# Kernel optimization log

Hardware: AMD Instinct MI355X
Metric: run time of the kernel (lower is better)

The kernel has to match this reference:

```python
import jax, jax.numpy as jnp
import numpy as np

B, N, C, H = 2, 2048, 1024, 16
D = C // H


def setup_inputs() -> dict:
    key = jax.random.key(0)
    k1, k2, k3, k4 = jax.random.split(key, 4)
    q = jax.random.normal(k1, (B, N, C), dtype=jnp.float32)
    k = jax.random.normal(k2, (B, H, N, D), dtype=jnp.float32)
    v = jax.random.normal(k3, (B, H, N, D), dtype=jnp.float32)
    # nn.Linear(C, C): weight [out, in], kaiming-uniform-ish scale
    proj_w = jax.random.normal(k4, (C, C), dtype=jnp.float32) * (1.0 / np.sqrt(C))
    proj_b = jnp.zeros((C,), dtype=jnp.float32)
    return {"q": q, "k": k, "v": v, "proj_w": proj_w, "proj_b": proj_b}


def reference(q, k, v, proj_w, proj_b):
    b, n, c = q.shape
    # [b,n,c] -> [b,h,n,d]
    qh = q.reshape(b, n, H, D).transpose(0, 2, 1, 3)
    # NOTE: original module has NO 1/sqrt(d) scaling — kept faithful.
    atten = jnp.einsum("bhnd,bhmd->bhnm", qh, k)
    atten = jax.nn.softmax(atten, axis=-1)
    # dropout layers are identity at inference
    x = jnp.einsum("bhnm,bhmd->bhnd", atten, v)
    x = x.transpose(0, 2, 1, 3).reshape(b, n, c)
    x = x @ proj_w.T + proj_b
    return x
```

## Files before the change

kernel.cpp:

```cpp
#include <hip/hip_runtime.h>
#include <hip/hip_bf16.h>

#define NB 2
#define NN 2048
#define NC 1024
#define NH 16
#define ND 64
#define LOG2E 1.4426950408889634f
#define NSPLIT 2

typedef __attribute__((ext_vector_type(4))) float f32x4;
typedef __attribute__((ext_vector_type(16))) float f32x16;
typedef __attribute__((ext_vector_type(8))) short bf16x8;
typedef __attribute__((ext_vector_type(4))) unsigned short us4;
typedef __attribute__((ext_vector_type(8))) unsigned short us8;
typedef __attribute__((ext_vector_type(4))) unsigned int u32x4;

#define MFMA32 __builtin_amdgcn_mfma_f32_32x32x16_bf16
#define MFMA16 __builtin_amdgcn_mfma_f32_16x16x32_bf16

#if __has_builtin(__builtin_amdgcn_exp2f)
#define EX2(x) __builtin_amdgcn_exp2f(x)
#else
#define EX2(x) __builtin_exp2f(x)
#endif

__device__ __forceinline__ unsigned short f2bf(float f) {
    unsigned int u = __builtin_bit_cast(unsigned int, f);
    u = (u + 0x7FFFu + ((u >> 16) & 1u)) >> 16;
    return (unsigned short)u;
}
__device__ __forceinline__ float bf2f(unsigned short h) {
    return __builtin_bit_cast(float, (unsigned int)h << 16);
}
__device__ __forceinline__ unsigned short f2bf_hw(float f) {
    __hip_bfloat16 b = __float2bfloat16(f);
    unsigned short u;
    __builtin_memcpy(&u, &b, 2);
    return u;
}
__device__ __forceinline__ unsigned int pk2(float lo, float hi) {
    return (unsigned int)f2bf_hw(lo) | ((unsigned int)f2bf_hw(hi) << 16);
}

__global__ __launch_bounds__(256) void kvf_kernel(const float* __restrict__ k,
                                                  const float* __restrict__ v,
                                                  unsigned short* __restrict__ kf,
                                                  unsigned short* __restrict__ vf) {
    __shared__ float T[32][68];
    const int bh = blockIdx.y, c = blockIdx.x, t = threadIdx.x;
    {
        const int row = t >> 3;
        const int g = t & 7;
        const float* src = k + ((size_t)bh * NN + c * 32 + row) * ND + g * 8;
        f32x4 x0 = *reinterpret_cast<const f32x4*>(src);
        f32x4 x1 = *reinterpret_cast<const f32x4*>(src + 4);
        us8 h;
        #pragma unroll
        for (int j = 0; j < 4; ++j) {
            h[j] = f2bf(x0[j]);
            h[4 + j] = f2bf(x1[j]);
        }
        const size_t fo = ((size_t)bh * 64 + c) * 2048 + g * 256 + row * 8;
        *reinterpret_cast<us8*>(kf + fo) = h;
    }
    {
        const int row = t >> 3, d0 = (t & 7) * 8;
        const float* src = v + ((size_t)bh * NN + c * 32 + row) * ND + d0;
        f32x4 a = *reinterpret_cast<const f32x4*>(src);
        f32x4 b2 = *reinterpret_cast<const f32x4*>(src + 4);
        *reinterpret_cast<f32x4*>(&T[row][d0]) = a;
        *reinterpret_cast<f32x4*>(&T[row][d0 + 4]) = b2;
    }
    __syncthreads();
    {
        const int g2 = t >> 6, hi = (t >> 5) & 1, l31 = t & 31;
        const int ks2 = g2 & 1, dt = g2 >> 1;
        us8 r;
        #pragma unroll
        for (int j = 0; j < 8; ++j) r[j] = f2bf(T[ks2 * 16 + hi * 8 + j][dt * 32 + l31]);
        const size_t fo = ((size_t)bh * 64 + c) * 2048 + (g2 * 2 + hi) * 256 + l31 * 8;
        *reinterpret_cast<us8*>(vf + fo) = r;
    }
}

__global__ __launch_bounds__(256) void wf_kernel(const float* __restrict__ w,
                                                 unsigned short* __restrict__ wf) {
    const int tid = blockIdx.x * 256 + threadIdx.x;
    const int ot = tid >> 11;
    const int s = tid & 2047;
    const int cc = s >> 6;
    const int lane = s & 63;
    const int l15 = lane & 15, lhi = lane >> 4;
    const float* src = w + (size_t)(ot * 16 + l15) * NC + cc * 32 + lhi * 8;
    f32x4 x0 = *reinterpret_cast<const f32x4*>(src);
    f32x4 x1 = *reinterpret_cast<const f32x4*>(src + 4);
    us8 r;
    #pragma unroll
    for (int j = 0; j < 4; ++j) {
        r[j] = f2bf(x0[j]);
        r[4 + j] = f2bf(x1[j]);
    }
    *reinterpret_cast<us8*>(wf + (size_t)tid * 8) = r;
}

#define ATTN_STEP(KC, KN, VC, VN, CI, CN)                                              \
    {                                                                                  \
        _Pragma("unroll")                                                              \
        for (int ks = 0; ks < 4; ++ks)                                                 \
            KN[ks] = *reinterpret_cast<const bf16x8*>(Kp + (CN) * 2048 + ks * 512);    \
        _Pragma("unroll")                                                              \
        for (int g = 0; g < 4; ++g)                                                    \
            VN[g] = *reinterpret_cast<const bf16x8*>(Vp + (CN) * 2048 + g * 512);      \
        f32x16 sa;                                                                     \
        _Pragma("unroll")                                                              \
        for (int r = 0; r < 16; ++r) sa[r] = 0.f;                                      \
        _Pragma("unroll")                                                              \
        for (int ks = 0; ks < 4; ++ks) sa = MFMA32(KC[ks], qh[ks], sa, 0, 0, 0);       \
        _Pragma("unroll")                                                              \
        for (int r = 0; r < 16; r += 4) {                                              \
            float e0 = EX2(sa[r]);                                                     \
            float e1 = EX2(sa[r + 1]);                                                 \
            float e2 = EX2(sa[r + 2]);                                                 \
            float e3 = EX2(sa[r + 3]);                                                 \
            sa[r] = e0; sa[r + 1] = e1; sa[r + 2] = e2; sa[r + 3] = e3;                \
            rs0 += e0; rs1 += e1; rs2 += e2; rs3 += e3;                                \
        }                                                                              \
        _Pragma("unroll")                                                              \
        for (int ks2 = 0; ks2 < 2; ++ks2) {                                            \
            unsigned int sA = pk2(sa[8 * ks2 + 0], sa[8 * ks2 + 1]);                   \
            unsigned int sB = pk2(sa[8 * ks2 + 2], sa[8 * ks2 + 3]);                   \
            unsigned int sC = pk2(sa[8 * ks2 + 4], sa[8 * ks2 + 5]);                   \
            unsigned int sD = pk2(sa[8 * ks2 + 6], sa[8 * ks2 + 7]);                   \
            unsigned int snd0 = hi ? sA : sC;                                          \
            unsigned int snd1 = hi ? sB : sD;                                          \
            unsigned int rcv0 = __shfl_xor(snd0, 32);                                  \
            unsigned int rcv1 = __shfl_xor(snd1, 32);                                  \
            u32x4 uf;                                                                  \
            uf[0] = hi ? rcv0 : sA;                                                    \
            uf[1] = hi ? rcv1 : sB;                                                    \
            uf[2] = hi ? sC : rcv0;                                                    \
            uf[3] = hi ? sD : rcv1;                                                    \
            bf16x8 pfrag = __builtin_bit_cast(bf16x8, uf);                             \
            if (ks2 == 0) {                                                            \
                acc0 = MFMA32(VC[0], pfrag, acc0, 0, 0, 0);                            \
                acc1 = MFMA32(VC[2], pfrag, acc1, 0, 0, 0);                            \
            } else {                                                                   \
                acc0 = MFMA32(VC[1], pfrag, acc0, 0, 0, 0);                            \
                acc1 = MFMA32(VC[3], pfrag, acc1, 0, 0, 0);                            \
            }                                                                          \
        }                                                                              \
    }

__global__ __launch_bounds__(256, 2) void attn_kernel(const float* __restrict__ q,
                                                      const unsigned short* __restrict__ kf,
                                                      const unsigned short* __restrict__ vf,
                                                      unsigned short* __restrict__ po,
                                                      float* __restrict__ pl) {
    const size_t X_ELEMS = (size_t)NB * NN * NC;
    const size_t ML_ELEMS = (size_t)NB * NN * NH;
    const int bid = blockIdx.x;
    const int swz = (bid & 7) * 128 + (bid >> 3);
    const int bh = swz >> 5;
    const int qt = (swz & 31) >> 1;
    const int split = swz & 1;
    const int b = bh >> 4, h = bh & 15;
    const int wave = threadIdx.x >> 6, lane = threadIdx.x & 63;
    const int l31 = lane & 31, hi = lane >> 5;
    const int qrow = qt * 128 + wave * 32 + l31;

    bf16x8 qh[4];
    {
        const float* qp = q + ((size_t)(b * NN + qrow)) * NC + h * ND;
        #pragma unroll
        for (int ks = 0; ks < 4; ++ks) {
            int d = ks * 16 + hi * 8;
            f32x4 x0 = *reinterpret_cast<const f32x4*>(qp + d);
            f32x4 x1 = *reinterpret_cast<const f32x4*>(qp + d + 4);
            bf16x8 ah;
            #pragma unroll
            for (int j = 0; j < 4; ++j) {
                ah[j] = (short)f2bf_hw(x0[j] * LOG2E);
                ah[4 + j] = (short)f2bf_hw(x1[j] * LOG2E);
            }
            qh[ks] = ah;
        }
    }

    f32x16 acc0, acc1;
    #pragma unroll
    for (int r = 0; r < 16; ++r) { acc0[r] = 0.f; acc1[r] = 0.f; }
    float rs0 = 0.f, rs1 = 0.f, rs2 = 0.f, rs3 = 0.f;

    const unsigned short* Kp = kf + (size_t)(bh * 64 + split * 32) * 2048 + hi * 256 + l31 * 8;
    const unsigned short* Vp = vf + (size_t)(bh * 64 + split * 32) * 2048 + hi * 256 + l31 * 8;

    bf16x8 kA[4], kB[4], vA[4], vB[4];
    #pragma unroll
    for (int ks = 0; ks < 4; ++ks) {
        kA[ks] = *reinterpret_cast<const bf16x8*>(Kp + ks * 512);
        vA[ks] = *reinterpret_cast<const bf16x8*>(Vp + ks * 512);
    }

    for (int ci = 0; ci < 32; ci += 2) {
        ATTN_STEP(kA, kB, vA, vB, ci, ci + 1)
        const int cn2 = (ci < 30) ? ci + 2 : 31;
        ATTN_STEP(kB, kA, vB, vA, ci + 1, cn2)
    }

    float rs = (rs0 + rs1) + (rs2 + rs3);
    rs += __shfl_xor(rs, 32);
    const float inv = 1.0f / rs;

    unsigned short* pob = po + (size_t)split * X_ELEMS;
    float* plb = pl + (size_t)split * ML_ELEMS;
    const int el15 = l31 & 15;
    const int nt = b * 128 + qt * 8 + wave * 2 + (l31 >> 4);
    #pragma unroll
    for (int dt = 0; dt < 2; ++dt) {
        const f32x16 a = (dt == 0) ? acc0 : acc1;
        unsigned int P0 = pk2(a[0] * inv, a[1] * inv);
        unsigned int P1 = pk2(a[2] * inv, a[3] * inv);
        unsigned int P2 = pk2(a[4] * inv, a[5] * inv);
        unsigned int P3 = pk2(a[6] * inv, a[7] * inv);
        unsigned int P4 = pk2(a[8] * inv, a[9] * inv);
        unsigned int P5 = pk2(a[10] * inv, a[11] * inv);
        unsigned int P6 = pk2(a[12] * inv, a[13] * inv);
        unsigned int P7 = pk2(a[14] * inv, a[15] * inv);
        unsigned int r0 = __shfl_xor(hi ? P0 : P4, 32);
        unsigned int r1 = __shfl_xor(hi ? P1 : P5, 32);
        unsigned int r2 = __shfl_xor(hi ? P2 : P6, 32);
        unsigned int r3 = __shfl_xor(hi ? P3 : P7, 32);
        u32x4 c0, c1;
        c0[0] = hi ? r0 : P0;
        c0[1] = hi ? r1 : P1;
        c0[2] = hi ? P4 : r0;
        c0[3] = hi ? P5 : r1;
        c1[0] = hi ? r2 : P2;
        c1[1] = hi ? r3 : P3;
        c1[2] = hi ? P6 : r2;
        c1[3] = hi ? P7 : r3;
        unsigned short* base = pob + (size_t)(nt * 32 + h * 2 + dt) * 512;
        *reinterpret_cast<u32x4*>(base + (hi * 32 + el15) * 8) = c0;
        *reinterpret_cast<u32x4*>(base + (hi * 32 + 16 + el15) * 8) = c1;
    }
    if (hi == 0) {
        plb[(size_t)(b * NN + qrow) * NH + h] = rs;
    }
}

__global__ __launch_bounds__(256) void combine_kernel(const unsigned short* __restrict__ po,
                                                      const float* __restrict__ pl,
                                                      unsigned short* __restrict__ xf) {
    const size_t X_ELEMS = (size_t)NB * NN * NC;
    const size_t ML_ELEMS = (size_t)NB * NN * NH;
    const int tid = blockIdx.x * 256 + threadIdx.x;
    const int nt = tid >> 10;
    const int v = tid & 1023;
    const int h = v >> 6;
    const int lane = v & 63;
    const int row = nt * 16 + (lane & 15);
    float w[NSPLIT];
    {
        float lsum = 0.f;
        #pragma unroll
        for (int i = 0; i < NSPLIT; ++i) {
            w[i] = pl[(size_t)i * ML_ELEMS + (size_t)row * NH + h];
            lsum += w[i];
        }
        float inv = 1.0f / lsum;
        #pragma unroll
        for (int i = 0; i < NSPLIT; ++i) w[i] *= inv;
    }
    const size_t s0 = (size_t)(nt * 32 + h * 2) * 512 + lane * 8;
    const size_t s1 = s0 + 512;
    float f0[8], f1[8];
    #pragma unroll
    for (int j = 0; j < 8; ++j) { f0[j] = 0.f; f1[j] = 0.f; }
    #pragma unroll
    for (int i = 0; i < NSPLIT; ++i) {
        us8 e0 = *reinterpret_cast<const us8*>(po + (size_t)i * X_ELEMS + s0);
        us8 e1 = *reinterpret_cast<const us8*>(po + (size_t)i * X_ELEMS + s1);
        #pragma unroll
        for (int j = 0; j < 8; ++j) {
            f0[j] += w[i] * bf2f(e0[j]);
            f1[j] += w[i] * bf2f(e1[j]);
        }
    }
    us8 o0_, o1_;
    #pragma unroll
    for (int j = 0; j < 8; ++j) {
        o0_[j] = f2bf_hw(f0[j]);
        o1_[j] = f2bf_hw(f1[j]);
    }
    *reinterpret_cast<us8*>(xf + s0) = o0_;
    *reinterpret_cast<us8*>(xf + s1) = o1_;
}

__global__ __launch_bounds__(256, 2) void proj_kernel(const unsigned short* __restrict__ xf,
                                                      const unsigned short* __restrict__ wf,
                                                      const float* __restrict__ bias,
                                                      float* __restrict__ out) {
    const int bid = blockIdx.x;
    const int swz = (bid & 7) * 64 + (bid >> 3);
    const int bx = swz >> 4;
    const int by = swz & 15;
    const int wave = threadIdx.x >> 6, lane = threadIdx.x & 63;
    const int l15 = lane & 15, lhi = lane >> 4;
    const int nt0 = bx * 8 + wave * 2;
    const int ot0 = by * 4;

    const unsigned short* xA = xf + (size_t)nt0 * 32 * 512 + lane * 8;
    const unsigned short* xB = xA + 32 * 512;
    const unsigned short* wB = wf + (size_t)ot0 * 32 * 512 + lane * 8;

    f32x4 acc[2][4];
    #pragma unroll
    for (int g = 0; g < 2; ++g)
        #pragma unroll
        for (int c = 0; c < 4; ++c) acc[g][c] = (f32x4){0.f, 0.f, 0.f, 0.f};

    bf16x8 a0 = *reinterpret_cast<const bf16x8*>(xA);
    bf16x8 a1 = *reinterpret_cast<const bf16x8*>(xB);
    bf16x8 bfr[4];
    #pragma unroll
    for (int cb = 0; cb < 4; ++cb)
        bfr[cb] = *reinterpret_cast<const bf16x8*>(wB + (size_t)cb * 32 * 512);

    for (int cc = 0; cc < 32; ++cc) {
        const int ccn = (cc < 31) ? cc + 1 : 31;
        bf16x8 a0n = *reinterpret_cast<const bf16x8*>(xA + (size_t)ccn * 512);
        bf16x8 a1n = *reinterpret_cast<const bf16x8*>(xB + (size_t)ccn * 512);
        bf16x8 bn[4];
        #pragma unroll
        for (int cb = 0; cb < 4; ++cb)
            bn[cb] = *reinterpret_cast<const bf16x8*>(wB + (size_t)(cb * 32 + ccn) * 512);
        #pragma unroll
        for (int cb = 0; cb < 4; ++cb) {
            acc[0][cb] = MFMA16(a0, bfr[cb], acc[0][cb], 0, 0, 0);
            acc[1][cb] = MFMA16(a1, bfr[cb], acc[1][cb], 0, 0, 0);
        }
        a0 = a0n; a1 = a1n;
        #pragma unroll
        for (int cb = 0; cb < 4; ++cb) bfr[cb] = bn[cb];
    }
    #pragma unroll
    for (int g = 0; g < 2; ++g)
        #pragma unroll
        for (int cb = 0; cb < 4; ++cb)
            #pragma unroll
            for (int v = 0; v < 4; ++v) {
                int n = bx * 128 + wave * 32 + g * 16 + lhi * 4 + v;
                int o = by * 64 + cb * 16 + l15;
                out[(size_t)n * NC + o] = acc[g][cb][v] + bias[o];
            }
}

extern "C" void kernel_launch(void* const* d_in, const int* in_sizes, int n_in,
                              void* d_out, int out_size, void* d_ws, size_t ws_size,
                              hipStream_t stream) {
    const float* q    = (const float*)d_in[0];
    const float* k    = (const float*)d_in[1];
    const float* v    = (const float*)d_in[2];
    const float* w    = (const float*)d_in[3];
    const float* bias = (const float*)d_in[4];
    float* out = (float*)d_out;

    const size_t KV_ELEMS = (size_t)NB * NH * NN * ND;
    const size_t X_ELEMS  = (size_t)NB * NN * NC;
    const size_t W_ELEMS  = (size_t)NC * NC;
    const size_t ML_ELEMS = (size_t)NB * NN * NH;

    unsigned short* kfb = (unsigned short*)d_ws;
    unsigned short* vfb = kfb + KV_ELEMS;
    unsigned short* wfb = vfb + KV_ELEMS;
    unsigned short* pob = wfb + W_ELEMS;
    unsigned short* xfb = pob + (size_t)NSPLIT * X_ELEMS;
    float* plb = (float*)(xfb + X_ELEMS);

    dim3 fg(NN / 32, NB * NH);
    kvf_kernel<<<fg, 256, 0, stream>>>(k, v, kfb, vfb);
    wf_kernel<<<512, 256, 0, stream>>>(w, wfb);

    attn_kernel<<<1024, 256, 0, stream>>>(q, kfb, vfb, pob, plb);
    combine_kernel<<<1024, 256, 0, stream>>>(pob, plb, xfb);

    proj_kernel<<<512, 256, 0, stream>>>(xfb, wfb, bias, out);
}
```

Before: 104.1 us.

## Stage K/V tiles in double-buffered LDS shared across waves, split KV four ways

The attention kernel now copies each K/V chunk once per block into double-buffered shared memory with direct global-to-LDS loads. All four waves read it from there, instead of each wave fetching the same K/V from global memory into registers. The KV sequence split rises from 2 to 4 and the attention grid doubles, which adds parallelism but writes more partial outputs for the combine step. Each chunk iteration now needs a block barrier, which can stall waves.

```diff
diff --git a/kernel.cpp b/kernel.cpp
--- a/kernel.cpp
+++ b/kernel.cpp
@@ -7,7 +7,7 @@
 #define NH 16
 #define ND 64
 #define LOG2E 1.4426950408889634f
-#define NSPLIT 2
+#define NSPLIT 4
 
 typedef __attribute__((ext_vector_type(4))) float f32x4;
 typedef __attribute__((ext_vector_type(16))) float f32x16;
@@ -24,6 +24,12 @@
 #else
 #define EX2(x) __builtin_exp2f(x)
 #endif
+
+__device__ __forceinline__ void load_lds16(const unsigned short* g, unsigned short* l) {
+    __builtin_amdgcn_global_load_lds(
+        (const __attribute__((address_space(1))) unsigned int*)g,
+        (__attribute__((address_space(3))) unsigned int*)l, 16, 0, 0);
+}
 
 __device__ __forceinline__ unsigned short f2bf(float f) {
     unsigned int u = __builtin_bit_cast(unsigned int, f);
@@ -104,68 +110,23 @@
     *reinterpret_cast<us8*>(wf + (size_t)tid * 8) = r;
 }
 
-#define ATTN_STEP(KC, KN, VC, VN, CI, CN)                                              \
-    {                                                                                  \
-        _Pragma("unroll")                                                              \
-        for (int ks = 0; ks < 4; ++ks)                                                 \
-            KN[ks] = *reinterpret_cast<const bf16x8*>(Kp + (CN) * 2048 + ks * 512);    \
-        _Pragma("unroll")                                                              \
-        for (int g = 0; g < 4; ++g)                                                    \
-            VN[g] = *reinterpret_cast<const bf16x8*>(Vp + (CN) * 2048 + g * 512);      \
-        f32x16 sa;                                                                     \
-        _Pragma("unroll")                                                              \
-        for (int r = 0; r < 16; ++r) sa[r] = 0.f;                                      \
-        _Pragma("unroll")                                                              \
-        for (int ks = 0; ks < 4; ++ks) sa = MFMA32(KC[ks], qh[ks], sa, 0, 0, 0);       \
-        _Pragma("unroll")                                                              \
-        for (int r = 0; r < 16; r += 4) {                                              \
-            float e0 = EX2(sa[r]);                                                     \
-            float e1 = EX2(sa[r + 1]);                                                 \
-            float e2 = EX2(sa[r + 2]);                                                 \
-            float e3 = EX2(sa[r + 3]);                                                 \
-            sa[r] = e0; sa[r + 1] = e1; sa[r + 2] = e2; sa[r + 3] = e3;                \
-            rs0 += e0; rs1 += e1; rs2 += e2; rs3 += e3;                                \
-        }                                                                              \
-        _Pragma("unroll")                                                              \
-        for (int ks2 = 0; ks2 < 2; ++ks2) {                                            \
-            unsigned int sA = pk2(sa[8 * ks2 + 0], sa[8 * ks2 + 1]);                   \
-            unsigned int sB = pk2(sa[8 * ks2 + 2], sa[8 * ks2 + 3]);                   \
-            unsigned int sC = pk2(sa[8 * ks2 + 4], sa[8 * ks2 + 5]);                   \
-            unsigned int sD = pk2(sa[8 * ks2 + 6], sa[8 * ks2 + 7]);                   \
-            unsigned int snd0 = hi ? sA : sC;                                          \
-            unsigned int snd1 = hi ? sB : sD;                                          \
-            unsigned int rcv0 = __shfl_xor(snd0, 32);                                  \
-            unsigned int rcv1 = __shfl_xor(snd1, 32);                                  \
-            u32x4 uf;                                                                  \
-            uf[0] = hi ? rcv0 : sA;                                                    \
-            uf[1] = hi ? rcv1 : sB;                                                    \
-            uf[2] = hi ? sC : rcv0;                                                    \
-            uf[3] = hi ? sD : rcv1;                                                    \
-            bf16x8 pfrag = __builtin_bit_cast(bf16x8, uf);                             \
-            if (ks2 == 0) {                                                            \
-                acc0 = MFMA32(VC[0], pfrag, acc0, 0, 0, 0);                            \
-                acc1 = MFMA32(VC[2], pfrag, acc1, 0, 0, 0);                            \
-            } else {                                                                   \
-                acc0 = MFMA32(VC[1], pfrag, acc0, 0, 0, 0);                            \
-                acc1 = MFMA32(VC[3], pfrag, acc1, 0, 0, 0);                            \
-            }                                                                          \
-        }                                                                              \
-    }
-
 __global__ __launch_bounds__(256, 2) void attn_kernel(const float* __restrict__ q,
                                                       const unsigned short* __restrict__ kf,
                                                       const unsigned short* __restrict__ vf,
                                                       unsigned short* __restrict__ po,
                                                       float* __restrict__ pl) {
+    __shared__ __align__(16) unsigned short sK[2][2048];
+    __shared__ __align__(16) unsigned short sV[2][2048];
     const size_t X_ELEMS = (size_t)NB * NN * NC;
     const size_t ML_ELEMS = (size_t)NB * NN * NH;
     const int bid = blockIdx.x;
-    const int swz = (bid & 7) * 128 + (bid >> 3);
-    const int bh = swz >> 5;
-    const int qt = (swz & 31) >> 1;
-    const int split = swz & 1;
+    const int swz = (bid & 7) * 256 + (bid >> 3);
+    const int bh = swz >> 6;
+    const int qt = (swz >> 2) & 15;
+    const int split = swz & 3;
     const int b = bh >> 4, h = bh & 15;
-    const int wave = threadIdx.x >> 6, lane = threadIdx.x & 63;
+    const int t = threadIdx.x;
+    const int wave = t >> 6, lane = t & 63;
     const int l31 = lane & 31, hi = lane >> 5;
     const int qrow = qt * 128 + wave * 32 + l31;
 
@@ -192,20 +153,64 @@
     for (int r = 0; r < 16; ++r) { acc0[r] = 0.f; acc1[r] = 0.f; }
     float rs0 = 0.f, rs1 = 0.f, rs2 = 0.f, rs3 = 0.f;
 
-    const unsigned short* Kp = kf + (size_t)(bh * 64 + split * 32) * 2048 + hi * 256 + l31 * 8;
-    const unsigned short* Vp = vf + (size_t)(bh * 64 + split * 32) * 2048 + hi * 256 + l31 * 8;
-
-    bf16x8 kA[4], kB[4], vA[4], vB[4];
-    #pragma unroll
-    for (int ks = 0; ks < 4; ++ks) {
-        kA[ks] = *reinterpret_cast<const bf16x8*>(Kp + ks * 512);
-        vA[ks] = *reinterpret_cast<const bf16x8*>(Vp + ks * 512);
-    }
-
-    for (int ci = 0; ci < 32; ci += 2) {
-        ATTN_STEP(kA, kB, vA, vB, ci, ci + 1)
-        const int cn2 = (ci < 30) ? ci + 2 : 31;
-        ATTN_STEP(kB, kA, vB, vA, ci + 1, cn2)
+    const unsigned short* KpT = kf + (size_t)(bh * 64 + split * 16) * 2048 + (size_t)t * 8;
+    const unsigned short* VpT = vf + (size_t)(bh * 64 + split * 16) * 2048 + (size_t)t * 8;
+    const int fo = hi * 256 + l31 * 8;
+
+    load_lds16(KpT, &sK[0][wave * 512]);
+    load_lds16(VpT, &sV[0][wave * 512]);
+    __syncthreads();
+
+    for (int ci = 0; ci < 16; ++ci) {
+        const int bb = ci & 1;
+        if (ci < 15) {
+            load_lds16(KpT + (size_t)(ci + 1) * 2048, &sK[bb ^ 1][wave * 512]);
+            load_lds16(VpT + (size_t)(ci + 1) * 2048, &sV[bb ^ 1][wave * 512]);
+        }
+        const unsigned short* Kb = &sK[bb][fo];
+        const unsigned short* Vb = &sV[bb][fo];
+
+        f32x16 sa;
+        #pragma unroll
+        for (int r = 0; r < 16; ++r) sa[r] = 0.f;
+        #pragma unroll
+        for (int ks = 0; ks < 4; ++ks) {
+            bf16x8 kk = *reinterpret_cast<const bf16x8*>(Kb + ks * 512);
+            sa = MFMA32(kk, qh[ks], sa, 0, 0, 0);
+        }
+
+        #pragma unroll
+        for (int r = 0; r < 16; r += 4) {
+            float e0 = EX2(sa[r]);
+            float e1 = EX2(sa[r + 1]);
+            float e2 = EX2(sa[r + 2]);
+            float e3 = EX2(sa[r + 3]);
+            sa[r] = e0; sa[r + 1] = e1; sa[r + 2] = e2; sa[r + 3] = e3;
+            rs0 += e0; rs1 += e1; rs2 += e2; rs3 += e3;
+        }
+
+        #pragma unroll
+        for (int ks2 = 0; ks2 < 2; ++ks2) {
+            unsigned int sA = pk2(sa[8 * ks2 + 0], sa[8 * ks2 + 1]);
+            unsigned int sB = pk2(sa[8 * ks2 + 2], sa[8 * ks2 + 3]);
+            unsigned int sC = pk2(sa[8 * ks2 + 4], sa[8 * ks2 + 5]);
+            unsigned int sD = pk2(sa[8 * ks2 + 6], sa[8 * ks2 + 7]);
+            unsigned int snd0 = hi ? sA : sC;
+            unsigned int snd1 = hi ? sB : sD;
+            unsigned int rcv0 = __shfl_xor(snd0, 32);
+            unsigned int rcv1 = __shfl_xor(snd1, 32);
+            u32x4 uf;
+            uf[0] = hi ? rcv0 : sA;
+            uf[1] = hi ? rcv1 : sB;
+            uf[2] = hi ? sC : rcv0;
+            uf[3] = hi ? sD : rcv1;
+            bf16x8 pfrag = __builtin_bit_cast(bf16x8, uf);
+            bf16x8 v0 = *reinterpret_cast<const bf16x8*>(Vb + (0 * 2 + ks2) * 512);
+            bf16x8 v1 = *reinterpret_cast<const bf16x8*>(Vb + (1 * 2 + ks2) * 512);
+            acc0 = MFMA32(v0, pfrag, acc0, 0, 0, 0);
+            acc1 = MFMA32(v1, pfrag, acc1, 0, 0, 0);
+        }
+        __syncthreads();
     }
 
     float rs = (rs0 + rs1) + (rs2 + rs3);
@@ -382,7 +387,7 @@
     kvf_kernel<<<fg, 256, 0, stream>>>(k, v, kfb, vfb);
     wf_kernel<<<512, 256, 0, stream>>>(w, wfb);
 
-    attn_kernel<<<1024, 256, 0, stream>>>(q, kfb, vfb, pob, plb);
+    attn_kernel<<<2048, 256, 0, stream>>>(q, kfb, vfb, pob, plb);
     combine_kernel<<<1024, 256, 0, stream>>>(pob, plb, xfb);
 
     proj_kernel<<<512, 256, 0, stream>>>(xfb, wfb, bias, out);
```

Result: faster. 96.22 us (-7.6%).

## Stage K/V tiles through LDS with async global_load_lds triple buffering

Applied to the files above, without the earlier changes.

Replaces the per-wave register double-buffered global loads of K and V fragments with a shared triple-buffered LDS pipeline. Each thread issues a direct global-to-LDS load, the block waits on vmcnt and a barrier, and all four waves then read their fragments from LDS. This removes redundant global/L2 traffic, since every wave previously fetched the same K/V chunk itself. The cost is a block barrier per chunk and extra LDS reads. It also swaps the bf16 pack helper for the single v_cvt_pk_bf16_f32 instruction and adds an inline-asm exp2 fallback.

```diff
diff --git a/kernel.cpp b/kernel.cpp
--- a/kernel.cpp
+++ b/kernel.cpp
@@ -22,8 +22,19 @@
 #if __has_builtin(__builtin_amdgcn_exp2f)
 #define EX2(x) __builtin_amdgcn_exp2f(x)
 #else
-#define EX2(x) __builtin_exp2f(x)
+__device__ __forceinline__ float ex2_asm(float x) {
+    float r;
+    asm volatile("v_exp_f32 %0, %1\n\ts_nop 1" : "=v"(r) : "v"(x));
+    return r;
+}
+#define EX2(x) ex2_asm(x)
 #endif
+
+__device__ __forceinline__ void load_lds16(const unsigned short* g, unsigned short* l) {
+    __builtin_amdgcn_global_load_lds(
+        (const __attribute__((address_space(1))) unsigned int*)g,
+        (__attribute__((address_space(3))) unsigned int*)l, 16, 0, 0);
+}
 
 __device__ __forceinline__ unsigned short f2bf(float f) {
     unsigned int u = __builtin_bit_cast(unsigned int, f);
@@ -40,7 +51,9 @@
     return u;
 }
 __device__ __forceinline__ unsigned int pk2(float lo, float hi) {
-    return (unsigned int)f2bf_hw(lo) | ((unsigned int)f2bf_hw(hi) << 16);
+    unsigned int r;
+    asm("v_cvt_pk_bf16_f32 %0, %1, %2" : "=v"(r) : "v"(lo), "v"(hi));
+    return r;
 }
 
 __global__ __launch_bounds__(256) void kvf_kernel(const float* __restrict__ k,
@@ -104,19 +117,25 @@
     *reinterpret_cast<us8*>(wf + (size_t)tid * 8) = r;
 }
 
-#define ATTN_STEP(KC, KN, VC, VN, CI, CN)                                              \
+#define STAGE(CI, BUF)                                                   \
+    {                                                                    \
+        load_lds16(KpT + (size_t)(CI) * 2048, &sK[BUF][wave * 512]);     \
+        load_lds16(VpT + (size_t)(CI) * 2048, &sV[BUF][wave * 512]);     \
+    }
+
+#define ATTN_ITER(CI, CUR, NXT2)                                                       \
     {                                                                                  \
-        _Pragma("unroll")                                                              \
-        for (int ks = 0; ks < 4; ++ks)                                                 \
-            KN[ks] = *reinterpret_cast<const bf16x8*>(Kp + (CN) * 2048 + ks * 512);    \
-        _Pragma("unroll")                                                              \
-        for (int g = 0; g < 4; ++g)                                                    \
-            VN[g] = *reinterpret_cast<const bf16x8*>(Vp + (CN) * 2048 + g * 512);      \
+        if ((CI) < 30) STAGE((CI) + 2, NXT2);                                          \
+        const unsigned short* Kb = &sK[CUR][fo];                                       \
+        const unsigned short* Vb = &sV[CUR][fo];                                       \
         f32x16 sa;                                                                     \
         _Pragma("unroll")                                                              \
         for (int r = 0; r < 16; ++r) sa[r] = 0.f;                                      \
         _Pragma("unroll")                                                              \
-        for (int ks = 0; ks < 4; ++ks) sa = MFMA32(KC[ks], qh[ks], sa, 0, 0, 0);       \
+        for (int ks = 0; ks < 4; ++ks) {                                               \
+            bf16x8 kk = *reinterpret_cast<const bf16x8*>(Kb + ks * 512);               \
+            sa = MFMA32(kk, qh[ks], sa, 0, 0, 0);                                      \
+        }                                                                              \
         _Pragma("unroll")                                                              \
         for (int r = 0; r < 16; r += 4) {                                              \
             float e0 = EX2(sa[r]);                                                     \
@@ -142,13 +161,15 @@
             uf[2] = hi ? sC : rcv0;                                                    \
             uf[3] = hi ? sD : rcv1;                                                    \
             bf16x8 pfrag = __builtin_bit_cast(bf16x8, uf);                             \
-            if (ks2 == 0) {                                                            \
-                acc0 = MFMA32(VC[0], pfrag, acc0, 0, 0, 0);                            \
-                acc1 = MFMA32(VC[2], pfrag, acc1, 0, 0, 0);                            \
-            } else {                                                                   \
-                acc0 = MFMA32(VC[1], pfrag, acc0, 0, 0, 0);                            \
-                acc1 = MFMA32(VC[3], pfrag, acc1, 0, 0, 0);                            \
-            }                                                                          \
+            bf16x8 v0 = *reinterpret_cast<const bf16x8*>(Vb + (0 * 2 + ks2) * 512);    \
+            bf16x8 v1 = *reinterpret_cast<const bf16x8*>(Vb + (1 * 2 + ks2) * 512);    \
+            acc0 = MFMA32(v0, pfrag, acc0, 0, 0, 0);                                   \
+            acc1 = MFMA32(v1, pfrag, acc1, 0, 0, 0);                                   \
+        }                                                                              \
+        if ((CI) < 31) {                                                               \
+            if ((CI) == 30) asm volatile("s_waitcnt vmcnt(0)" ::: "memory");           \
+            else            asm volatile("s_waitcnt vmcnt(2)" ::: "memory");           \
+            __builtin_amdgcn_s_barrier();                                              \
         }                                                                              \
     }
 
@@ -157,6 +178,8 @@
                                                       const unsigned short* __restrict__ vf,
                                                       unsigned short* __restrict__ po,
                                                       float* __restrict__ pl) {
+    __shared__ __align__(16) unsigned short sK[3][2048];
+    __shared__ __align__(16) unsigned short sV[3][2048];
     const size_t X_ELEMS = (size_t)NB * NN * NC;
     const size_t ML_ELEMS = (size_t)NB * NN * NH;
     const int bid = blockIdx.x;
@@ -165,7 +188,8 @@
     const int qt = (swz & 31) >> 1;
     const int split = swz & 1;
     const int b = bh >> 4, h = bh & 15;
-    const int wave = threadIdx.x >> 6, lane = threadIdx.x & 63;
+    const int t = threadIdx.x;
+    const int wave = t >> 6, lane = t & 63;
     const int l31 = lane & 31, hi = lane >> 5;
     const int qrow = qt * 128 + wave * 32 + l31;
 
@@ -192,21 +216,22 @@
     for (int r = 0; r < 16; ++r) { acc0[r] = 0.f; acc1[r] = 0.f; }
     float rs0 = 0.f, rs1 = 0.f, rs2 = 0.f, rs3 = 0.f;
 
-    const unsigned short* Kp = kf + (size_t)(bh * 64 + split * 32) * 2048 + hi * 256 + l31 * 8;
-    const unsigned short* Vp = vf + (size_t)(bh * 64 + split * 32) * 2048 + hi * 256 + l31 * 8;
-
-    bf16x8 kA[4], kB[4], vA[4], vB[4];
-    #pragma unroll
-    for (int ks = 0; ks < 4; ++ks) {
-        kA[ks] = *reinterpret_cast<const bf16x8*>(Kp + ks * 512);
-        vA[ks] = *reinterpret_cast<const bf16x8*>(Vp + ks * 512);
-    }
-
-    for (int ci = 0; ci < 32; ci += 2) {
-        ATTN_STEP(kA, kB, vA, vB, ci, ci + 1)
-        const int cn2 = (ci < 30) ? ci + 2 : 31;
-        ATTN_STEP(kB, kA, vB, vA, ci + 1, cn2)
-    }
+    const unsigned short* KpT = kf + (size_t)(bh * 64 + split * 32) * 2048 + (size_t)t * 8;
+    const unsigned short* VpT = vf + (size_t)(bh * 64 + split * 32) * 2048 + (size_t)t * 8;
+    const int fo = hi * 256 + l31 * 8;
+
+    STAGE(0, 0)
+    STAGE(1, 1)
+    asm volatile("s_waitcnt vmcnt(2)" ::: "memory");
+    __builtin_amdgcn_s_barrier();
+
+    for (int base = 0; base < 30; base += 3) {
+        ATTN_ITER(base, 0, 2)
+        ATTN_ITER(base + 1, 1, 0)
+        ATTN_ITER(base + 2, 2, 1)
+    }
+    ATTN_ITER(30, 0, 2)
+    ATTN_ITER(31, 1, 0)
 
     float rs = (rs0 + rs1) + (rs2 + rs3);
     rs += __shfl_xor(rs, 32);
@@ -240,9 +265,9 @@
         c1[1] = hi ? r3 : P3;
         c1[2] = hi ? P6 : r2;
         c1[3] = hi ? P7 : r3;
-        unsigned short* base = pob + (size_t)(nt * 32 + h * 2 + dt) * 512;
-        *reinterpret_cast<u32x4*>(base + (hi * 32 + el15) * 8) = c0;
-        *reinterpret_cast<u32x4*>(base + (hi * 32 + 16 + el15) * 8) = c1;
+        unsigned short* base_ = pob + (size_t)(nt * 32 + h * 2 + dt) * 512;
+        *reinterpret_cast<u32x4*>(base_ + (hi * 32 + el15) * 8) = c0;
+        *reinterpret_cast<u32x4*>(base_ + (hi * 32 + 16 + el15) * 8) = c1;
     }
     if (hi == 0) {
         plb[(size_t)(b * NN + qrow) * NH + h] = rs;
```

New measurement: 90.13 us. 13.4% less time.
